# Optimization experiments

Measured on AMD Instinct MI355X. Metric: run time of the kernel, lower is better.

## Reference

```python
import jax, jax.numpy as jnp
import numpy as np

EPS = 1e-6
NUM_HEADS = 16
ROPE_THETA = 100000.0


def _rope_tables(seq_len, head_dim, theta):
    inv_freq = 1.0 / (theta ** (np.arange(0, head_dim, 2, dtype=np.float32) / head_dim))
    t = np.arange(seq_len, dtype=np.float32)
    freqs = np.outer(t, inv_freq)                      # (S, head_dim//2)
    emb = np.concatenate([freqs, freqs], axis=-1)      # (S, head_dim)
    return jnp.asarray(np.cos(emb))[None], jnp.asarray(np.sin(emb))[None]  # (1,S,D)


def setup_inputs() -> dict:
    key = jax.random.key(0)
    ks = jax.random.split(key, 6)
    B, S, H = 2, 2048, 1024
    head_dim = H // NUM_HEADS
    cos, sin = _rope_tables(S, head_dim, ROPE_THETA)
    scale = 0.02
    return {
        "hidden_states": jax.random.normal(ks[0], (B, S, H), dtype=jnp.float32),
        "cos": cos, "sin": sin,
        "Wq": jax.random.normal(ks[1], (H, H), dtype=jnp.float32) * scale,
        "bq": jnp.zeros((H,), dtype=jnp.float32),
        "Wk": jax.random.normal(ks[2], (H, H), dtype=jnp.float32) * scale,
        "bk": jnp.zeros((H,), dtype=jnp.float32),
        "Wv": jax.random.normal(ks[3], (H, H), dtype=jnp.float32) * scale,
        "bv": jnp.zeros((H,), dtype=jnp.float32),
        "Wo": jax.random.normal(ks[4], (H, H), dtype=jnp.float32) * scale,
        "bo": jnp.zeros((H,), dtype=jnp.float32),
        "rms_weight": jnp.ones((H,), dtype=jnp.float32),
    }


def _rms_norm(x, w):
    var = jnp.mean(x * x, axis=-1, keepdims=True)
    return x * jax.lax.rsqrt(var + EPS) * w


def _rotate_half(x):
    x1, x2 = jnp.split(x, 2, axis=-1)
    return jnp.concatenate([-x2, x1], axis=-1)


def reference(hidden_states, cos, sin, Wq, bq, Wk, bk, Wv, bv, Wo, bo, rms_weight):
    B, S, H = hidden_states.shape
    D = H // NUM_HEADS
    q = hidden_states @ Wq.T + bq
    k = hidden_states @ Wk.T + bk
    v = hidden_states @ Wv.T + bv
    # RMSNorm over full hidden dim BEFORE head split (as in original)
    q = _rms_norm(q, rms_weight)
    k = _rms_norm(k, rms_weight)
    # (B,S,H) -> (B,heads,S,D)
    q = q.reshape(B, S, NUM_HEADS, D).transpose(0, 2, 1, 3)
    k = k.reshape(B, S, NUM_HEADS, D).transpose(0, 2, 1, 3)
    v = v.reshape(B, S, NUM_HEADS, D).transpose(0, 2, 1, 3)
    # RoPE: cos/sin (1,S,D) -> unsqueeze head dim
    c = cos[:, None, :, :]
    s = sin[:, None, :, :]
    q = q * c + _rotate_half(q) * s
    k = k * c + _rotate_half(k) * s
    # attention (faithful: boolean tril mask is ADDED as 0/1, not -inf)
    scale = D ** 0.5
    scores = jnp.einsum("bhqd,bhkd->bhqk", q, k) / scale
    mask = jnp.tril(jnp.ones((S, S), dtype=scores.dtype))  # +1 on causal, +0 elsewhere
    attn = jax.nn.softmax(scores + mask, axis=-1)
    out = jnp.einsum("bhqk,bhkd->bhqd", attn, v)
    out = out.transpose(0, 2, 1, 3).reshape(B, S, H)
    return out @ Wo.T + bo
```

## Files before the change

kernel.cpp:

```cpp
#include <hip/hip_runtime.h>

typedef unsigned short u16;
typedef __attribute__((ext_vector_type(8))) _Float16 half8;
typedef __attribute__((ext_vector_type(2))) __fp16 fp16x2;
typedef __attribute__((ext_vector_type(4))) float f32x4;
typedef __attribute__((ext_vector_type(16))) float f32x16;

#define MFMAH(A,B,C) __builtin_amdgcn_mfma_f32_16x16x32_f16(A,B,C,0,0,0)
#define MFMA32(A,B,C) __builtin_amdgcn_mfma_f32_32x32x16_f16(A,B,C,0,0,0)
#define LOG2E 1.4426950408889634f
#define C1 0.18033688011112042f

__device__ __forceinline__ u16 f2h(float f){
  _Float16 h = (_Float16)f; u16 r; __builtin_memcpy(&r,&h,2); return r;
}
__device__ __forceinline__ float h2f(u16 v){
  _Float16 h; __builtin_memcpy(&h,&v,2); return (float)h;
}
__device__ __forceinline__ unsigned int pack_h2(float a, float b){
  fp16x2 h = __builtin_amdgcn_cvt_pkrtz(a,b);
  unsigned int r; __builtin_memcpy(&r,&h,4); return r;
}

__device__ __forceinline__ void async_ld16(const void* g, void* l) {
  __builtin_amdgcn_global_load_lds(
      (const __attribute__((address_space(1))) unsigned int*)g,
      (__attribute__((address_space(3))) unsigned int*)l, 16, 0, 0);
}

__global__ __launch_bounds__(256) void cast_all(const float* __restrict__ hs,
    const float* __restrict__ wq, const float* __restrict__ wk,
    const float* __restrict__ wv, const float* __restrict__ wo,
    u16* __restrict__ dst)
{
  unsigned int i = blockIdx.x*256 + threadIdx.x;
  size_t el = (size_t)i * 8;
  const float* src; size_t off;
  if (el < 4194304) { src = hs; off = el; }
  else {
    unsigned int r = (unsigned int)((el - 4194304) >> 20);
    src = (r==0)?wq:(r==1)?wk:(r==2)?wv:wo;
    off = (el - 4194304) & 1048575;
  }
  float4 a = *reinterpret_cast<const float4*>(src+off);
  float4 b = *reinterpret_cast<const float4*>(src+off+4);
  uint4 o = {pack_h2(a.x,a.y), pack_h2(a.z,a.w), pack_h2(b.x,b.y), pack_h2(b.z,b.w)};
  *reinterpret_cast<uint4*>(dst + el) = o;
}

__global__ __launch_bounds__(256) void gemm_qkv(const u16* __restrict__ A,
                                                const u16* __restrict__ W,
                                                const float* __restrict__ bqp,
                                                const float* __restrict__ bkp,
                                                const float* __restrict__ bvp,
                                                u16* __restrict__ qout,
                                                u16* __restrict__ kout,
                                                u16* __restrict__ vout,
                                                int M, int K)
{
  __shared__ __align__(16) u16 lds_a[128*32];
  __shared__ __align__(16) u16 lds_w[128*32];
  const int t = threadIdx.x;
  const int lane = t & 63, wave = t >> 6;
  const int wm = wave >> 1, wn = wave & 1;
  const int lr = lane & 15, quad = lane >> 4;
  const int flat = blockIdx.x;
  const int xcd = flat & 7, slot = flat >> 3;
  const int ln = slot % 12, lm = slot / 12;
  const int n0 = ((xcd & 1) * 12 + ln) * 128;
  const int m0 = ((xcd >> 1) * 8 + lm) * 128;
  const int wbase = t & 192;
  const int which = n0 >> 10;

  const f32x4 fzero = {0.f,0.f,0.f,0.f};
  f32x4 acc[4][4];
  #pragma unroll
  for (int i=0;i<4;++i)
    #pragma unroll
    for (int j=0;j<4;++j) acc[i][j] = fzero;

  if (which < 2) {
    for (int k0 = 0; k0 < K; k0 += 32) {
      __syncthreads();
      #pragma unroll
      for (int it=0; it<2; ++it) {
        int idx = it*256 + t;
        int row = idx >> 2, c8 = (idx & 3) * 8;
        int lbase = (it*256 + wbase) * 8;
        async_ld16(&A[(size_t)(m0+row)*K + k0 + c8], &lds_a[lbase]);
        async_ld16(&W[(size_t)(n0+row)*K + k0 + c8], &lds_w[lbase]);
      }
      __syncthreads();
      half8 af[4], bfr[4];
      #pragma unroll
      for (int mt=0; mt<4; ++mt)
        af[mt] = *reinterpret_cast<const half8*>(&lds_a[(wm*64 + mt*16 + lr)*32 + quad*8]);
      #pragma unroll
      for (int nt=0; nt<4; ++nt)
        bfr[nt] = *reinterpret_cast<const half8*>(&lds_w[(wn*64 + nt*16 + lr)*32 + quad*8]);
      #pragma unroll
      for (int mt=0; mt<4; ++mt)
        #pragma unroll
        for (int nt=0; nt<4; ++nt)
          acc[mt][nt] = MFMAH(bfr[nt], af[mt], acc[mt][nt]);
    }
    const float* bp = which ? bkp : bqp;
    u16* dst = which ? kout : qout;
    #pragma unroll
    for (int nt=0; nt<4; ++nt) {
      int nn = (n0 & 1023) + wn*64 + nt*16 + quad*4;
      float4 bv = *reinterpret_cast<const float4*>(&bp[nn]);
      int hh = nn >> 6, d4 = nn & 63;
      #pragma unroll
      for (int mt=0; mt<4; ++mt) {
        int m = m0 + wm*64 + mt*16 + lr;
        int b = m >> 11, s = m & 2047;
        uint2 o = {pack_h2(acc[mt][nt][0]+bv.x, acc[mt][nt][1]+bv.y),
                   pack_h2(acc[mt][nt][2]+bv.z, acc[mt][nt][3]+bv.w)};
        *reinterpret_cast<uint2*>(&dst[((size_t)(b*16 + hh)*2048 + s)*64 + d4]) = o;
      }
    }
  } else {
    for (int k0 = 0; k0 < K; k0 += 32) {
      __syncthreads();
      #pragma unroll
      for (int it=0; it<2; ++it) {
        int idx = it*256 + t;
        int row = idx >> 2, c8 = (idx & 3) * 8;
        int lbase = (it*256 + wbase) * 8;
        async_ld16(&A[(size_t)(m0+row)*K + k0 + c8], &lds_a[lbase]);
        async_ld16(&W[(size_t)(n0+row)*K + k0 + c8], &lds_w[lbase]);
      }
      __syncthreads();
      half8 af[4], bfr[4];
      #pragma unroll
      for (int mt=0; mt<4; ++mt)
        af[mt] = *reinterpret_cast<const half8*>(&lds_a[(wm*64 + mt*16 + lr)*32 + quad*8]);
      #pragma unroll
      for (int nt=0; nt<4; ++nt)
        bfr[nt] = *reinterpret_cast<const half8*>(&lds_w[(wn*64 + nt*16 + lr)*32 + quad*8]);
      #pragma unroll
      for (int mt=0; mt<4; ++mt)
        #pragma unroll
        for (int nt=0; nt<4; ++nt)
          acc[mt][nt] = MFMAH(af[mt], bfr[nt], acc[mt][nt]);
    }
    #pragma unroll
    for (int nt=0; nt<4; ++nt) {
      int nn = (n0 & 1023) + wn*64 + nt*16 + lr;
      float bv = bvp[nn];
      int hh = nn >> 6, d = nn & 63;
      #pragma unroll
      for (int mt=0; mt<4; ++mt) {
        int m = m0 + wm*64 + mt*16 + quad*4;
        int b = m >> 11, s = m & 2047;
        uint2 o = {pack_h2(acc[mt][nt][0]+bv, acc[mt][nt][1]+bv),
                   pack_h2(acc[mt][nt][2]+bv, acc[mt][nt][3]+bv)};
        *reinterpret_cast<uint2*>(&vout[((size_t)(b*16 + hh)*64 + d)*2048 + s]) = o;
      }
    }
  }
}

__global__ __launch_bounds__(256) void gemm_o(const u16* __restrict__ A,
                                              const u16* __restrict__ W,
                                              const float* __restrict__ bias,
                                              float* __restrict__ O,
                                              int M, int N, int K)
{
  __shared__ __align__(16) u16 lds_a[128*32];
  __shared__ __align__(16) u16 lds_w[64*32];
  const int t = threadIdx.x;
  const int lane = t & 63, wm = t >> 6;
  const int lr = lane & 15, quad = lane >> 4;
  const int flat = blockIdx.x;
  const int xcd = flat & 7, slot = flat >> 3;
  const int n0 = (slot & 15) * 64;
  const int m0 = ((xcd << 2) + (slot >> 4)) * 128;
  const int wbase = t & 192;

  const f32x4 fzero = {0.f,0.f,0.f,0.f};
  f32x4 acc[2][4];
  #pragma unroll
  for (int i=0;i<2;++i)
    #pragma unroll
    for (int j=0;j<4;++j) acc[i][j] = fzero;

  for (int k0 = 0; k0 < K; k0 += 32) {
    __syncthreads();
    #pragma unroll
    for (int it=0; it<2; ++it) {
      int idx = it*256 + t;
      int row = idx >> 2, c8 = (idx & 3) * 8;
      int lbase = (it*256 + wbase) * 8;
      async_ld16(&A[(size_t)(m0+row)*K + k0 + c8], &lds_a[lbase]);
    }
    async_ld16(&W[(size_t)(n0 + (t>>2))*K + k0 + (t&3)*8], &lds_w[wbase*8]);
    __syncthreads();
    half8 af[2], bfr[4];
    #pragma unroll
    for (int mt=0; mt<2; ++mt)
      af[mt] = *reinterpret_cast<const half8*>(&lds_a[(wm*32 + mt*16 + lr)*32 + quad*8]);
    #pragma unroll
    for (int nt=0; nt<4; ++nt)
      bfr[nt] = *reinterpret_cast<const half8*>(&lds_w[(nt*16 + lr)*32 + quad*8]);
    #pragma unroll
    for (int mt=0; mt<2; ++mt)
      #pragma unroll
      for (int nt=0; nt<4; ++nt)
        acc[mt][nt] = MFMAH(bfr[nt], af[mt], acc[mt][nt]);
  }

  #pragma unroll
  for (int nt=0; nt<4; ++nt) {
    int nb = n0 + nt*16 + quad*4;
    float4 bv = *reinterpret_cast<const float4*>(&bias[nb]);
    #pragma unroll
    for (int mt=0; mt<2; ++mt) {
      int m = m0 + wm*32 + mt*16 + lr;
      float4 o = {acc[mt][nt][0]+bv.x, acc[mt][nt][1]+bv.y,
                  acc[mt][nt][2]+bv.z, acc[mt][nt][3]+bv.w};
      *reinterpret_cast<float4*>(&O[(size_t)m * N + nb]) = o;
    }
  }
}

__global__ __launch_bounds__(128) void rmsrope(u16* __restrict__ qb, u16* __restrict__ kb,
                                               const float* __restrict__ cosb,
                                               const float* __restrict__ sinb,
                                               const float* __restrict__ w)
{
  u16* buf = blockIdx.y ? kb : qb;
  const int bs = blockIdx.x;
  const int b = bs >> 11, s = bs & 2047;
  const int t = threadIdx.x;
  const int h = t >> 3, d0 = (t & 7) * 4;
  size_t base = ((size_t)(b*16+h)*2048 + s)*64;

  uint2 u1 = *reinterpret_cast<const uint2*>(&buf[base + d0]);
  uint2 u2 = *reinterpret_cast<const uint2*>(&buf[base + d0 + 32]);
  u16 a1[4], a2[4];
  __builtin_memcpy(a1, &u1, 8); __builtin_memcpy(a2, &u2, 8);
  float x1[4], x2[4];
  float ss = 0.f;
  #pragma unroll
  for (int j=0;j<4;++j){
    x1[j] = h2f(a1[j]); x2[j] = h2f(a2[j]);
    ss += x1[j]*x1[j] + x2[j]*x2[j];
  }
  #pragma unroll
  for (int off=32; off>0; off>>=1) ss += __shfl_xor(ss, off, 64);
  __shared__ float red[2];
  if ((t & 63) == 0) red[t>>6] = ss;
  __syncthreads();
  float tot = red[0] + red[1];
  float r = rsqrtf(tot * (1.0f/1024.0f) + 1e-6f);

  float4 w1 = *reinterpret_cast<const float4*>(&w[h*64+d0]);
  float4 w2 = *reinterpret_cast<const float4*>(&w[h*64+d0+32]);
  float4 c1 = *reinterpret_cast<const float4*>(&cosb[s*64+d0]);
  float4 s1 = *reinterpret_cast<const float4*>(&sinb[s*64+d0]);
  float4 c2 = *reinterpret_cast<const float4*>(&cosb[s*64+d0+32]);
  float4 s2 = *reinterpret_cast<const float4*>(&sinb[s*64+d0+32]);
  float n1[4] = {x1[0]*r*w1.x, x1[1]*r*w1.y, x1[2]*r*w1.z, x1[3]*r*w1.w};
  float n2[4] = {x2[0]*r*w2.x, x2[1]*r*w2.y, x2[2]*r*w2.z, x2[3]*r*w2.w};
  float o1[4] = {n1[0]*c1.x - n2[0]*s1.x, n1[1]*c1.y - n2[1]*s1.y,
                 n1[2]*c1.z - n2[2]*s1.z, n1[3]*c1.w - n2[3]*s1.w};
  float o2[4] = {n2[0]*c2.x + n1[0]*s2.x, n2[1]*c2.y + n1[1]*s2.y,
                 n2[2]*c2.z + n1[2]*s2.z, n2[3]*c2.w + n1[3]*s2.w};
  uint2 v1 = {pack_h2(o1[0],o1[1]), pack_h2(o1[2],o1[3])};
  uint2 v2 = {pack_h2(o2[0],o2[1]), pack_h2(o2[2],o2[3])};
  *reinterpret_cast<uint2*>(&buf[base + d0])      = v1;
  *reinterpret_cast<uint2*>(&buf[base + d0 + 32]) = v2;
}

__global__ __launch_bounds__(256) void attn(const u16* __restrict__ qh,
                                            const u16* __restrict__ kh,
                                            const u16* __restrict__ vt,
                                            u16* __restrict__ ao)
{
  __shared__ __align__(16) u16 kbuf[2][64*72];
  __shared__ __align__(16) u16 vbuf[2][64*72];
  const int t = threadIdx.x;
  const int lane = t & 63, w = t >> 6;
  const int ql = lane & 31, hf = lane >> 5;
  const int flat = blockIdx.x;
  const int xcd = flat & 7, slot = flat >> 3;
  const int bh = xcd + ((slot >> 4) << 3);
  const int qbase = (slot & 15) * 128;
  const int b = bh >> 4, h = bh & 15;
  const size_t hb = (size_t)bh * 2048 * 64;
  const u16* qp = qh + hb;
  const u16* kp = kh + hb;
  const u16* vtp = vt + hb;

  const int q_abs = qbase + w*32 + ql;
  half8 qf[4];
  #pragma unroll
  for (int s=0;s<4;++s)
    qf[s] = *reinterpret_cast<const half8*>(&qp[(size_t)q_abs*64 + s*16 + hf*8]);

  half8 onesf;
  #pragma unroll
  for (int i=0;i<8;++i) onesf[i] = (_Float16)1.0f;

  const int row = t >> 3;
  const int cc = t & 7;
  const int base2 = 32*(cc>>2) + 16*((cc>>1)&1) + 4*(cc&1);
  const int kofs = row*72 + cc*8;
  const u16* kg = kp + (size_t)row*64 + cc*8;
  const u16* vg = vtp + (size_t)row*2048 + base2;

  const f32x16 fz16 = {0.f,0.f,0.f,0.f,0.f,0.f,0.f,0.f,0.f,0.f,0.f,0.f,0.f,0.f,0.f,0.f};
  f32x16 oacc[2];
  oacc[0] = fz16; oacc[1] = fz16;
  f32x16 lacc = fz16;
  const int diag = (qbase + w*32) >> 6;

  {
    uint4 k0v = *reinterpret_cast<const uint4*>(kg);
    uint4 k1v = *reinterpret_cast<const uint4*>(kg + 32*64);
    uint2 a0 = *reinterpret_cast<const uint2*>(vg);
    uint2 a1 = *reinterpret_cast<const uint2*>(vg + 8);
    uint2 b0 = *reinterpret_cast<const uint2*>(vg + (size_t)32*2048);
    uint2 b1 = *reinterpret_cast<const uint2*>(vg + (size_t)32*2048 + 8);
    *reinterpret_cast<uint4*>(&kbuf[0][kofs])        = k0v;
    *reinterpret_cast<uint4*>(&kbuf[0][kofs+32*72])  = k1v;
    uint4 v0 = {a0.x,a0.y,a1.x,a1.y};
    uint4 v1 = {b0.x,b0.y,b1.x,b1.y};
    *reinterpret_cast<uint4*>(&vbuf[0][kofs])        = v0;
    *reinterpret_cast<uint4*>(&vbuf[0][kofs+32*72])  = v1;
  }

  for (int kt=0; kt<32; ++kt) {
    uint4 k0n, k1n; uint2 a0n, a1n, b0n, b1n;
    if (kt < 31) {
      const u16* kgn = kg + (size_t)(kt+1)*4096;
      const u16* vgn = vg + (kt+1)*64;
      k0n = *reinterpret_cast<const uint4*>(kgn);
      k1n = *reinterpret_cast<const uint4*>(kgn + 32*64);
      a0n = *reinterpret_cast<const uint2*>(vgn);
      a1n = *reinterpret_cast<const uint2*>(vgn + 8);
      b0n = *reinterpret_cast<const uint2*>(vgn + (size_t)32*2048);
      b1n = *reinterpret_cast<const uint2*>(vgn + (size_t)32*2048 + 8);
    }
    __syncthreads();
    const u16* kb = kbuf[kt & 1];
    const u16* vb = vbuf[kt & 1];

    unsigned int pk[4][4];
    #pragma unroll
    for (int kh2=0; kh2<2; ++kh2) {
      f32x16 z = fz16;
      #pragma unroll
      for (int s=0;s<4;++s) {
        half8 kf;
        __builtin_memcpy(&kf, &kb[(kh2*32+ql)*72 + s*16 + hf*8], 16);
        z = MFMA32(kf, qf[s], z);
      }
      float p[16];
      if (kt != diag) {
        float ml = (kt < diag) ? LOG2E : 0.0f;
        #pragma unroll
        for (int r=0;r<16;++r)
          p[r] = __builtin_amdgcn_exp2f(__builtin_fmaf(z[r], C1, ml));
      } else {
        #pragma unroll
        for (int r=0;r<16;++r) {
          int key = kt*64 + kh2*32 + (r&3) + 8*(r>>2) + 4*hf;
          float ml = (key <= q_abs) ? LOG2E : 0.0f;
          p[r] = __builtin_amdgcn_exp2f(__builtin_fmaf(z[r], C1, ml));
        }
      }
      #pragma unroll
      for (int t2=0;t2<2;++t2)
        #pragma unroll
        for (int jj=0;jj<4;++jj)
          pk[kh2*2+t2][jj] = pack_h2(p[t2*8+jj*2], p[t2*8+jj*2+1]);
    }

    #pragma unroll
    for (int st=0;st<4;++st) {
      uint4 pq = {pk[st][0], pk[st][1], pk[st][2], pk[st][3]};
      half8 pf; __builtin_memcpy(&pf, &pq, 16);
      lacc = MFMA32(onesf, pf, lacc);
      #pragma unroll
      for (int dh=0; dh<2; ++dh) {
        half8 vf;
        __builtin_memcpy(&vf, &vb[(dh*32+ql)*72 + st*16 + hf*8], 16);
        oacc[dh] = MFMA32(vf, pf, oacc[dh]);
      }
    }

    if (kt < 31) {
      u16* kwn = &kbuf[(kt+1)&1][kofs];
      u16* vwn = &vbuf[(kt+1)&1][kofs];
      *reinterpret_cast<uint4*>(kwn)         = k0n;
      *reinterpret_cast<uint4*>(kwn + 32*72) = k1n;
      uint4 v0 = {a0n.x,a0n.y,a1n.x,a1n.y};
      uint4 v1 = {b0n.x,b0n.y,b1n.x,b1n.y};
      *reinterpret_cast<uint4*>(vwn)         = v0;
      *reinterpret_cast<uint4*>(vwn + 32*72) = v1;
    }
  }

  float inv = 1.0f / lacc[0];
  size_t rowbase = ((size_t)(b*2048 + q_abs))*1024 + h*64;
  #pragma unroll
  for (int dh=0; dh<2; ++dh)
    #pragma unroll
    for (int rq=0; rq<4; ++rq) {
      int dd = dh*32 + 8*rq + 4*hf;
      uint2 o = {pack_h2(oacc[dh][rq*4+0]*inv, oacc[dh][rq*4+1]*inv),
                 pack_h2(oacc[dh][rq*4+2]*inv, oacc[dh][rq*4+3]*inv)};
      *reinterpret_cast<uint2*>(&ao[rowbase + dd]) = o;
    }
}

extern "C" void kernel_launch(void* const* d_in, const int* in_sizes, int n_in,
                              void* d_out, int out_size, void* d_ws, size_t ws_size,
                              hipStream_t stream)
{
  const float* hs   = (const float*)d_in[0];
  const float* cosb = (const float*)d_in[1];
  const float* sinb = (const float*)d_in[2];
  const float* Wq   = (const float*)d_in[3];
  const float* bq   = (const float*)d_in[4];
  const float* Wk   = (const float*)d_in[5];
  const float* bk   = (const float*)d_in[6];
  const float* Wv   = (const float*)d_in[7];
  const float* bv   = (const float*)d_in[8];
  const float* Wo   = (const float*)d_in[9];
  const float* bo   = (const float*)d_in[10];
  const float* rw   = (const float*)d_in[11];

  const size_t NEL = (size_t)4096 * 1024;
  const size_t WEL = (size_t)1024 * 1024;
  u16* hsb = (u16*)d_ws;
  u16* wqb = hsb + NEL;
  u16* wob = wqb + 3*WEL;
  u16* qhb = wob + WEL;
  u16* khb = qhb + NEL;
  u16* vtb = khb + NEL;
  u16* aob = hsb;

  cast_all<<<4096, 256, 0, stream>>>(hs, Wq, Wk, Wv, Wo, hsb);
  gemm_qkv<<<768, 256, 0, stream>>>(hsb, wqb, bq, bk, bv, qhb, khb, vtb, 4096, 1024);
  rmsrope<<<dim3(4096,2), 128, 0, stream>>>(qhb, khb, cosb, sinb, rw);
  attn<<<512, 256, 0, stream>>>(qhb, khb, vtb, aob);
  gemm_o<<<512, 256, 0, stream>>>(aob, wob, bo, (float*)d_out, 4096, 1024, 1024);
}
```

Measured before the change: 219.3 us.

## Split attention key range across two wave groups and merge partial sums

Each attention block now runs 512 threads in two groups of four waves. Each group processes half of the key sequence with its own double-buffered K/V shared-memory tiles. The second group writes its unnormalized output accumulators and row sums to shared memory, and the first group adds them in before normalizing and storing. This halves the serial key loop per wave and doubles the waves in flight, at the cost of more shared memory per block, an extra exchange with two barriers, and fewer resident blocks per CU.

New measurement: 246.4 us. +12.3%, slower.

```diff
diff --git a/kernel.cpp b/kernel.cpp
--- a/kernel.cpp
+++ b/kernel.cpp
@@ -274,15 +274,16 @@
   *reinterpret_cast<uint2*>(&buf[base + d0 + 32]) = v2;
 }
 
-__global__ __launch_bounds__(256) void attn(const u16* __restrict__ qh,
-                                            const u16* __restrict__ kh,
-                                            const u16* __restrict__ vt,
-                                            u16* __restrict__ ao)
-{
-  __shared__ __align__(16) u16 kbuf[2][64*72];
-  __shared__ __align__(16) u16 vbuf[2][64*72];
+__global__ __launch_bounds__(512, 4) void attn(const u16* __restrict__ qh,
+                                               const u16* __restrict__ kh,
+                                               const u16* __restrict__ vt,
+                                               u16* __restrict__ ao)
+{
+  __shared__ __align__(16) u16 kbuf[2][2][64*72];
+  __shared__ __align__(16) u16 vbuf[2][2][64*72];
   const int t = threadIdx.x;
   const int lane = t & 63, w = t >> 6;
+  const int g = w >> 2, wq = w & 3;
   const int ql = lane & 31, hf = lane >> 5;
   const int flat = blockIdx.x;
   const int xcd = flat & 7, slot = flat >> 3;
@@ -294,7 +295,7 @@
   const u16* kp = kh + hb;
   const u16* vtp = vt + hb;
 
-  const int q_abs = qbase + w*32 + ql;
+  const int q_abs = qbase + wq*32 + ql;
   half8 qf[4];
   #pragma unroll
   for (int s=0;s<4;++s)
@@ -304,18 +305,19 @@
   #pragma unroll
   for (int i=0;i<8;++i) onesf[i] = (_Float16)1.0f;
 
-  const int row = t >> 3;
-  const int cc = t & 7;
+  const int lt = t & 255;
+  const int row = lt >> 3;
+  const int cc = lt & 7;
   const int base2 = 32*(cc>>2) + 16*((cc>>1)&1) + 4*(cc&1);
   const int kofs = row*72 + cc*8;
-  const u16* kg = kp + (size_t)row*64 + cc*8;
-  const u16* vg = vtp + (size_t)row*2048 + base2;
+  const u16* kg = kp + (size_t)(g*1024 + row)*64 + cc*8;
+  const u16* vg = vtp + (size_t)row*2048 + g*1024 + base2;
 
   const f32x16 fz16 = {0.f,0.f,0.f,0.f,0.f,0.f,0.f,0.f,0.f,0.f,0.f,0.f,0.f,0.f,0.f,0.f};
   f32x16 oacc[2];
   oacc[0] = fz16; oacc[1] = fz16;
   f32x16 lacc = fz16;
-  const int diag = (qbase + w*32) >> 6;
+  const int diag = (qbase + wq*32) >> 6;
 
   {
     uint4 k0v = *reinterpret_cast<const uint4*>(kg);
@@ -324,17 +326,17 @@
     uint2 a1 = *reinterpret_cast<const uint2*>(vg + 8);
     uint2 b0 = *reinterpret_cast<const uint2*>(vg + (size_t)32*2048);
     uint2 b1 = *reinterpret_cast<const uint2*>(vg + (size_t)32*2048 + 8);
-    *reinterpret_cast<uint4*>(&kbuf[0][kofs])        = k0v;
-    *reinterpret_cast<uint4*>(&kbuf[0][kofs+32*72])  = k1v;
+    *reinterpret_cast<uint4*>(&kbuf[g][0][kofs])        = k0v;
+    *reinterpret_cast<uint4*>(&kbuf[g][0][kofs+32*72])  = k1v;
     uint4 v0 = {a0.x,a0.y,a1.x,a1.y};
     uint4 v1 = {b0.x,b0.y,b1.x,b1.y};
-    *reinterpret_cast<uint4*>(&vbuf[0][kofs])        = v0;
-    *reinterpret_cast<uint4*>(&vbuf[0][kofs+32*72])  = v1;
-  }
-
-  for (int kt=0; kt<32; ++kt) {
+    *reinterpret_cast<uint4*>(&vbuf[g][0][kofs])        = v0;
+    *reinterpret_cast<uint4*>(&vbuf[g][0][kofs+32*72])  = v1;
+  }
+
+  for (int kt=0; kt<16; ++kt) {
     uint4 k0n, k1n; uint2 a0n, a1n, b0n, b1n;
-    if (kt < 31) {
+    if (kt < 15) {
       const u16* kgn = kg + (size_t)(kt+1)*4096;
       const u16* vgn = vg + (kt+1)*64;
       k0n = *reinterpret_cast<const uint4*>(kgn);
@@ -345,8 +347,9 @@
       b1n = *reinterpret_cast<const uint2*>(vgn + (size_t)32*2048 + 8);
     }
     __syncthreads();
-    const u16* kb = kbuf[kt & 1];
-    const u16* vb = vbuf[kt & 1];
+    const u16* kb = &kbuf[g][kt & 1][0];
+    const u16* vb = &vbuf[g][kt & 1][0];
+    const int gkt = (g << 4) + kt;
 
     unsigned int pk[4][4];
     #pragma unroll
@@ -359,15 +362,15 @@
         z = MFMA32(kf, qf[s], z);
       }
       float p[16];
-      if (kt != diag) {
-        float ml = (kt < diag) ? LOG2E : 0.0f;
+      if (gkt != diag) {
+        float ml = (gkt < diag) ? LOG2E : 0.0f;
         #pragma unroll
         for (int r=0;r<16;++r)
           p[r] = __builtin_amdgcn_exp2f(__builtin_fmaf(z[r], C1, ml));
       } else {
         #pragma unroll
         for (int r=0;r<16;++r) {
-          int key = kt*64 + kh2*32 + (r&3) + 8*(r>>2) + 4*hf;
+          int key = gkt*64 + kh2*32 + (r&3) + 8*(r>>2) + 4*hf;
           float ml = (key <= q_abs) ? LOG2E : 0.0f;
           p[r] = __builtin_amdgcn_exp2f(__builtin_fmaf(z[r], C1, ml));
         }
@@ -392,9 +395,9 @@
       }
     }
 
-    if (kt < 31) {
-      u16* kwn = &kbuf[(kt+1)&1][kofs];
-      u16* vwn = &vbuf[(kt+1)&1][kofs];
+    if (kt < 15) {
+      u16* kwn = &kbuf[g][(kt+1)&1][kofs];
+      u16* vwn = &vbuf[g][(kt+1)&1][kofs];
       *reinterpret_cast<uint4*>(kwn)         = k0n;
       *reinterpret_cast<uint4*>(kwn + 32*72) = k1n;
       uint4 v0 = {a0n.x,a0n.y,a1n.x,a1n.y};
@@ -404,17 +407,36 @@
     }
   }
 
-  float inv = 1.0f / lacc[0];
-  size_t rowbase = ((size_t)(b*2048 + q_abs))*1024 + h*64;
-  #pragma unroll
-  for (int dh=0; dh<2; ++dh)
-    #pragma unroll
-    for (int rq=0; rq<4; ++rq) {
-      int dd = dh*32 + 8*rq + 4*hf;
-      uint2 o = {pack_h2(oacc[dh][rq*4+0]*inv, oacc[dh][rq*4+1]*inv),
-                 pack_h2(oacc[dh][rq*4+2]*inv, oacc[dh][rq*4+3]*inv)};
-      *reinterpret_cast<uint2*>(&ao[rowbase + dd]) = o;
-    }
+  __syncthreads();
+  f32x4* xch4 = (f32x4*)&kbuf[0][0][0];
+  float* xls  = (float*)&vbuf[0][0][0];
+  const int idx = wq*64 + lane;
+  if (g == 1) {
+    #pragma unroll
+    for (int dh=0; dh<2; ++dh)
+      #pragma unroll
+      for (int rq=0; rq<4; ++rq) {
+        f32x4 v = {oacc[dh][rq*4+0], oacc[dh][rq*4+1],
+                   oacc[dh][rq*4+2], oacc[dh][rq*4+3]};
+        xch4[(dh*4+rq)*256 + idx] = v;
+      }
+    xls[idx] = lacc[0];
+  }
+  __syncthreads();
+  if (g == 0) {
+    float inv = 1.0f / (lacc[0] + xls[idx]);
+    size_t rowbase = ((size_t)(b*2048 + q_abs))*1024 + h*64;
+    #pragma unroll
+    for (int dh=0; dh<2; ++dh)
+      #pragma unroll
+      for (int rq=0; rq<4; ++rq) {
+        int dd = dh*32 + 8*rq + 4*hf;
+        f32x4 v = xch4[(dh*4+rq)*256 + idx];
+        uint2 o = {pack_h2((oacc[dh][rq*4+0]+v.x)*inv, (oacc[dh][rq*4+1]+v.y)*inv),
+                   pack_h2((oacc[dh][rq*4+2]+v.z)*inv, (oacc[dh][rq*4+3]+v.w)*inv)};
+        *reinterpret_cast<uint2*>(&ao[rowbase + dd]) = o;
+      }
+  }
 }
 
 extern "C" void kernel_launch(void* const* d_in, const int* in_sizes, int n_in,
@@ -447,6 +469,6 @@
   cast_all<<<4096, 256, 0, stream>>>(hs, Wq, Wk, Wv, Wo, hsb);
   gemm_qkv<<<768, 256, 0, stream>>>(hsb, wqb, bq, bk, bv, qhb, khb, vtb, 4096, 1024);
   rmsrope<<<dim3(4096,2), 128, 0, stream>>>(qhb, khb, cosb, sinb, rw);
-  attn<<<512, 256, 0, stream>>>(qhb, khb, vtb, aob);
+  attn<<<512, 512, 0, stream>>>(qhb, khb, vtb, aob);
   gemm_o<<<512, 256, 0, stream>>>(aob, wob, bo, (float*)d_out, 4096, 1024, 1024);
 }
```
